# Optimization experiments

Measured on AMD Instinct MI355X. Metric: run time of the kernel, lower is better.

## Reference

```python
import jax, jax.numpy as jnp
import numpy as np

D_IN = 1024
D_OUT = 1024


def setup_inputs() -> dict:
    key = jax.random.key(0)
    kx, kq, kk, kv = jax.random.split(key, 4)
    x = jax.random.normal(kx, (4, 2048, D_IN), dtype=jnp.float32)
    s = 1.0 / np.sqrt(D_IN)
    Wq = jax.random.normal(kq, (D_IN, D_OUT), dtype=jnp.float32) * s
    Wk = jax.random.normal(kk, (D_IN, D_OUT), dtype=jnp.float32) * s
    Wv = jax.random.normal(kv, (D_IN, D_OUT), dtype=jnp.float32) * s
    return {"x": x, "Wq": Wq, "Wk": Wk, "Wv": Wv}


def reference(x, Wq, Wk, Wv):
    # x: [b, s, d_in]; projections [b, s, d_out]
    q = jnp.einsum('bsd,de->bse', x, Wq)
    k = jnp.einsum('bsd,de->bse', x, Wk)
    v = jnp.einsum('bsd,de->bse', x, Wv)
    scale = 1.0 / jnp.sqrt(jnp.asarray(D_OUT, dtype=x.dtype))
    scores = jnp.einsum('bqe,bke->bqk', q, k) * scale  # [b, s, s]
    s_len = x.shape[1]
    causal = jnp.tril(jnp.ones((s_len, s_len), dtype=bool))
    scores = jnp.where(causal[None, :, :], scores, -jnp.inf)
    attn = jax.nn.softmax(scores, axis=-1)
    # dropout p=0.0 -> identity
    return jnp.einsum('bqk,bke->bqe', attn, v)
```

## Files before the change

### kernel.cpp

```cpp
#include <hip/hip_runtime.h>
#include <hip/hip_bf16.h>

#define S_LEN 2048
#define D_DIM 1024
#define NBATCH 4

typedef __attribute__((ext_vector_type(4)))  float f32x4;
typedef __attribute__((ext_vector_type(8)))  short s16x8;
typedef __attribute__((ext_vector_type(4)))  unsigned short u16x4;

__device__ __forceinline__ unsigned short f2b(float f) {
    __hip_bfloat16 h = __float2bfloat16(f);
    return __builtin_bit_cast(unsigned short, h);
}

__device__ __forceinline__ void load_lds16(const unsigned short* g, unsigned short* l) {
    __builtin_amdgcn_global_load_lds(
        (const __attribute__((address_space(1))) void*)(g),
        (__attribute__((address_space(3))) void*)(l), 16, 0, 0);
}

__global__ __launch_bounds__(256)
void cvt_kernel(const float* __restrict__ in, unsigned short* __restrict__ out) {
    long i = ((long)blockIdx.x * 256 + threadIdx.x) * 4;
    f32x4 v = *(const f32x4*)(in + i);
    u16x4 o;
    o.x = f2b(v.x); o.y = f2b(v.y); o.z = f2b(v.z); o.w = f2b(v.w);
    *(u16x4*)(out + i) = o;
}

__global__ __launch_bounds__(256)
void transW_kernel(const float* __restrict__ W0, const float* __restrict__ W1,
                   const float* __restrict__ W2, unsigned short* __restrict__ WT) {
    const float* W = (blockIdx.z == 0) ? W0 : (blockIdx.z == 1) ? W1 : W2;
    unsigned short* O = WT + (long)blockIdx.z * 1024 * 1024;
    __shared__ float t[32][33];
    int tid = threadIdx.x;
    int r  = tid >> 3;
    int c4 = tid & 7;
    int bi = blockIdx.x, bj = blockIdx.y;
    f32x4 v = *(const f32x4*)&W[(long)(bi * 32 + r) * 1024 + bj * 32 + c4 * 4];
    t[r][c4 * 4 + 0] = v.x; t[r][c4 * 4 + 1] = v.y;
    t[r][c4 * 4 + 2] = v.z; t[r][c4 * 4 + 3] = v.w;
    __syncthreads();
    u16x4 o;
    o.x = f2b(t[c4 * 4 + 0][r]); o.y = f2b(t[c4 * 4 + 1][r]);
    o.z = f2b(t[c4 * 4 + 2][r]); o.w = f2b(t[c4 * 4 + 3][r]);
    *(u16x4*)&O[(long)(bj * 32 + r) * 1024 + bi * 32 + c4 * 4] = o;
}

template<int BM, int BN, int OMODE, bool CSKIP, bool CKLIM>
__global__ __launch_bounds__(512, 2)
void gemm_big(const unsigned short* __restrict__ A, int lda, long aStride,
              const unsigned short* __restrict__ Bt, int ldb, long bStride,
              void* __restrict__ Cv, int ldc, long cStride,
              int K, float alpha) {
    constexpr int MF = BM / 32;
    constexpr int NF = BN / 64;
    constexpr int AI = BM / 64;
    constexpr int BI = BN / 64;
    const int bm = blockIdx.x, bn = blockIdx.y, bz = blockIdx.z;
    if (CSKIP && 2 * bn > bm) return;
    A  += (long)bz * aStride;
    Bt += (long)bz * bStride;

    const int tid  = threadIdx.x;
    const int lane = tid & 63;
    const int wid  = tid >> 6;
    const int wm   = wid >> 2;
    const int wn   = wid & 3;

    extern __shared__ __align__(16) unsigned short smem[];
    unsigned short* As = smem;
    unsigned short* Bs = smem + 2 * BM * 64;

    f32x4 acc[MF][NF] = {};

    const int kend = CKLIM ? (bm + 1) * BM : K;
    const int nt   = kend / 64;

    const int srl  = tid >> 3;
    const int sg   = (tid & 7) ^ (srl & 7);
    const int fr   = lane & 15;
    const int fg   = lane >> 4;
    const int rxor = (fr & 7) * 8;

    auto stage = [&](int g) {
        const int k0 = g * 64;
        unsigned short* da = As + (g & 1) * (BM * 64);
        #pragma unroll
        for (int i = 0; i < AI; ++i) {
            const int rl = i * 64 + srl;
            load_lds16(A + (long)(bm * BM + rl) * lda + k0 + sg * 8,
                       da + i * 4096 + wid * 512 + lane * 8);
        }
        unsigned short* db = Bs + (g & 1) * (BN * 64);
        #pragma unroll
        for (int i = 0; i < BI; ++i) {
            const int rl = i * 64 + srl;
            load_lds16(Bt + (long)(bn * BN + rl) * ldb + k0 + sg * 8,
                       db + i * 4096 + wid * 512 + lane * 8);
        }
    };

    stage(0);
    __syncthreads();

    for (int g = 0; g < nt; ++g) {
        if (g + 1 < nt) stage(g + 1);
        const unsigned short* as = As + (g & 1) * (BM * 64);
        const unsigned short* bs = Bs + (g & 1) * (BN * 64);
        #pragma unroll
        for (int ks = 0; ks < 2; ++ks) {
            s16x8 af[MF], bf[NF];
            #pragma unroll
            for (int m = 0; m < MF; ++m) {
                const int row = wm * (BM / 2) + m * 16 + fr;
                af[m] = *(const s16x8*)&as[row * 64 + (((ks * 4 + fg) * 8) ^ rxor)];
            }
            #pragma unroll
            for (int n = 0; n < NF; ++n) {
                const int row = wn * 64 + n * 16 + fr;
                bf[n] = *(const s16x8*)&bs[row * 64 + (((ks * 4 + fg) * 8) ^ rxor)];
            }
            __builtin_amdgcn_s_setprio(1);
            #pragma unroll
            for (int m = 0; m < MF; ++m)
                #pragma unroll
                for (int n = 0; n < NF; ++n)
                    acc[m][n] = __builtin_amdgcn_mfma_f32_16x16x32_bf16(af[m], bf[n], acc[m][n], 0, 0, 0);
            __builtin_amdgcn_s_setprio(0);
        }
        __syncthreads();
    }

    const int crow0 = bm * BM + wm * (BM / 2);
    const int ccol0 = bn * BN + wn * 64;
    const int cr = (lane >> 4) * 4;
    const int cc = lane & 15;
    if (OMODE == 0) {
        unsigned short* C = (unsigned short*)Cv + (long)bz * cStride;
        #pragma unroll
        for (int m = 0; m < MF; ++m)
            #pragma unroll
            for (int r = 0; r < 4; ++r) {
                const long row = crow0 + m * 16 + cr + r;
                #pragma unroll
                for (int n = 0; n < NF; ++n)
                    C[row * ldc + ccol0 + n * 16 + cc] = f2b(acc[m][n][r] * alpha);
            }
    } else {
        float* C = (float*)Cv + (long)bz * cStride;
        #pragma unroll
        for (int m = 0; m < MF; ++m)
            #pragma unroll
            for (int r = 0; r < 4; ++r) {
                const long row = crow0 + m * 16 + cr + r;
                #pragma unroll
                for (int n = 0; n < NF; ++n)
                    C[row * ldc + ccol0 + n * 16 + cc] = acc[m][n][r] * alpha;
            }
    }
}

__global__ __launch_bounds__(256)
void softmax_rows(float* __restrict__ scores) {
    const int i = blockIdx.x;
    const int z = blockIdx.y;
    float* row = scores + ((long)z * S_LEN + i) * S_LEN;
    const int c = i + 1;
    const int tid  = threadIdx.x;
    const int lane = tid & 63;
    const int wid  = tid >> 6;

    f32x4 v0 = ((const f32x4*)row)[tid];
    f32x4 v1 = ((const f32x4*)row)[tid + 256];
    const int j0 = tid * 4, j1 = (tid + 256) * 4;

    float m = -3.4e38f;
    #pragma unroll
    for (int e = 0; e < 4; e++) {
        if (j0 + e < c) m = fmaxf(m, v0[e]);
        if (j1 + e < c) m = fmaxf(m, v1[e]);
    }
    #pragma unroll
    for (int off = 32; off > 0; off >>= 1) m = fmaxf(m, __shfl_xor(m, off));
    __shared__ float redm[4];
    if (lane == 0) redm[wid] = m;
    __syncthreads();
    m = fmaxf(fmaxf(redm[0], redm[1]), fmaxf(redm[2], redm[3]));

    float e0[4], e1[4];
    float s = 0.f;
    #pragma unroll
    for (int e = 0; e < 4; e++) {
        e0[e] = (j0 + e < c) ? __expf(v0[e] - m) : 0.f;
        e1[e] = (j1 + e < c) ? __expf(v1[e] - m) : 0.f;
        s += e0[e] + e1[e];
    }
    #pragma unroll
    for (int off = 32; off > 0; off >>= 1) s += __shfl_xor(s, off);
    __shared__ float reds[4];
    if (lane == 0) reds[wid] = s;
    __syncthreads();
    s = reds[0] + reds[1] + reds[2] + reds[3];
    const float rinv = 1.f / s;

    unsigned short* P = (unsigned short*)row;
    u16x4 o0, o1;
    o0.x = f2b(e0[0] * rinv); o0.y = f2b(e0[1] * rinv);
    o0.z = f2b(e0[2] * rinv); o0.w = f2b(e0[3] * rinv);
    o1.x = f2b(e1[0] * rinv); o1.y = f2b(e1[1] * rinv);
    o1.z = f2b(e1[2] * rinv); o1.w = f2b(e1[3] * rinv);
    *(u16x4*)&P[j0] = o0;
    *(u16x4*)&P[j1] = o1;
}

extern "C" void kernel_launch(void* const* d_in, const int* in_sizes, int n_in,
                              void* d_out, int out_size, void* d_ws, size_t ws_size,
                              hipStream_t stream) {
    const float* x  = (const float*)d_in[0];
    const float* Wq = (const float*)d_in[1];
    const float* Wk = (const float*)d_in[2];
    const float* Wv = (const float*)d_in[3];
    float* out = (float*)d_out;
    char* ws = (char*)d_ws;
    const size_t MiB = 1ull << 20;

    unsigned short* xb  = (unsigned short*)(ws);
    unsigned short* WT  = (unsigned short*)(ws + 16 * MiB);
    unsigned short* Qb  = (unsigned short*)(ws + 22 * MiB);
    unsigned short* Kb  = (unsigned short*)(ws + 38 * MiB);
    unsigned short* VbT = (unsigned short*)(ws + 54 * MiB);
    float* scores       = (float*)(ws + 70 * MiB);

    int nb;
    if      (ws_size >= (70 + 64) * MiB) nb = 4;
    else if (ws_size >= (70 + 32) * MiB) nb = 2;
    else                                 nb = 1;

    const int LDS_QK = 2 * (256 + 256) * 64 * 2;
    const int LDS_SM = 2 * (128 + 256) * 64 * 2;
    hipFuncSetAttribute((const void*)gemm_big<256,256,0,false,false>,
                        hipFuncAttributeMaxDynamicSharedMemorySize, LDS_QK);
    hipFuncSetAttribute((const void*)gemm_big<128,256,0,false,false>,
                        hipFuncAttributeMaxDynamicSharedMemorySize, LDS_SM);
    hipFuncSetAttribute((const void*)gemm_big<128,256,1,true,false>,
                        hipFuncAttributeMaxDynamicSharedMemorySize, LDS_SM);
    hipFuncSetAttribute((const void*)gemm_big<128,256,1,false,true>,
                        hipFuncAttributeMaxDynamicSharedMemorySize, LDS_SM);

    cvt_kernel<<<8192, 256, 0, stream>>>(x, xb);
    transW_kernel<<<dim3(32, 32, 3), 256, 0, stream>>>(Wq, Wk, Wv, WT);

    gemm_big<256,256,0,false,false><<<dim3(32, 4, 2), 512, LDS_QK, stream>>>(
        xb, 1024, 0L, WT, 1024, (long)1024 * 1024,
        Qb, 1024, (long)8192 * 1024, 1024, 1.0f);
    gemm_big<128,256,0,false,false><<<dim3(8, 32, 1), 512, LDS_SM, stream>>>(
        WT + (long)2 * 1024 * 1024, 1024, 0L, xb, 1024, 0L,
        VbT, 8192, 0L, 1024, 1.0f);

    const float alpha = 0.03125f;
    for (int b0 = 0; b0 < NBATCH; b0 += nb) {
        const int nz = (NBATCH - b0 < nb) ? (NBATCH - b0) : nb;
        gemm_big<128,256,1,true,false><<<dim3(16, 8, nz), 512, LDS_SM, stream>>>(
            Qb + (long)b0 * S_LEN * D_DIM, 1024, (long)S_LEN * D_DIM,
            Kb + (long)b0 * S_LEN * D_DIM, 1024, (long)S_LEN * D_DIM,
            scores, S_LEN, (long)S_LEN * S_LEN, 1024, alpha);
        softmax_rows<<<dim3(S_LEN, nz), 256, 0, stream>>>(scores);
        gemm_big<128,256,1,false,true><<<dim3(16, 4, nz), 512, LDS_SM, stream>>>(
            (const unsigned short*)scores, 2 * S_LEN, 2L * S_LEN * S_LEN,
            VbT + (long)b0 * S_LEN, 8192, (long)S_LEN,
            out + (long)b0 * S_LEN * D_DIM, 1024, (long)S_LEN * D_DIM,
            S_LEN, 1.0f);
    }
}
```

Baseline: 242.9 us.

## Triple-buffer GEMM with vmcnt waits, fixed 128x256 tiles, reversed causal block order

Replaces the double-buffered GEMM with a single 128x256 tile kernel that uses a three-stage LDS ring. It waits on outstanding loads with explicit s_waitcnt vmcnt counts plus a single barrier per k-step instead of two syncthreads. The QKV projection moves from 256x256 to 128x256 tiles, and the causal kernels launch the heaviest row blocks first. The aim is deeper overlap of global-to-LDS loads with MFMA work and better load balance, at the cost of 144KB LDS per block, which can reduce occupancy.

Result: no change. 245.9 us (+1.3%).

```diff
diff --git a/kernel.cpp b/kernel.cpp
--- a/kernel.cpp
+++ b/kernel.cpp
@@ -49,17 +49,15 @@
     *(u16x4*)&O[(long)(bj * 32 + r) * 1024 + bi * 32 + c4 * 4] = o;
 }
 
-template<int BM, int BN, int OMODE, bool CSKIP, bool CKLIM>
+template<int OMODE, bool CSKIP, bool CKLIM>
 __global__ __launch_bounds__(512, 2)
-void gemm_big(const unsigned short* __restrict__ A, int lda, long aStride,
+void gemm_cnt(const unsigned short* __restrict__ A, int lda, long aStride,
               const unsigned short* __restrict__ Bt, int ldb, long bStride,
               void* __restrict__ Cv, int ldc, long cStride,
               int K, float alpha) {
-    constexpr int MF = BM / 32;
-    constexpr int NF = BN / 64;
-    constexpr int AI = BM / 64;
-    constexpr int BI = BN / 64;
-    const int bm = blockIdx.x, bn = blockIdx.y, bz = blockIdx.z;
+    constexpr int BUF = (128 + 256) * 64;
+    const int bm = (CSKIP || CKLIM) ? (gridDim.x - 1 - blockIdx.x) : blockIdx.x;
+    const int bn = blockIdx.y, bz = blockIdx.z;
     if (CSKIP && 2 * bn > bm) return;
     A  += (long)bz * aStride;
     Bt += (long)bz * bStride;
@@ -71,93 +69,90 @@
     const int wn   = wid & 3;
 
     extern __shared__ __align__(16) unsigned short smem[];
-    unsigned short* As = smem;
-    unsigned short* Bs = smem + 2 * BM * 64;
-
-    f32x4 acc[MF][NF] = {};
-
-    const int kend = CKLIM ? (bm + 1) * BM : K;
+
+    f32x4 acc[4][4] = {};
+
+    const int kend = CKLIM ? (bm + 1) * 128 : K;
     const int nt   = kend / 64;
 
-    const int srl  = tid >> 3;
-    const int sg   = (tid & 7) ^ (srl & 7);
+    const int srl = tid >> 3;
+    const int sg  = (tid & 7) ^ (srl & 7);
+    const unsigned short* agb = A  + (long)(bm * 128 + srl) * lda + sg * 8;
+    const unsigned short* bgb = Bt + (long)(bn * 256 + srl) * ldb + sg * 8;
+
     const int fr   = lane & 15;
     const int fg   = lane >> 4;
     const int rxor = (fr & 7) * 8;
 
-    auto stage = [&](int g) {
-        const int k0 = g * 64;
-        unsigned short* da = As + (g & 1) * (BM * 64);
-        #pragma unroll
-        for (int i = 0; i < AI; ++i) {
-            const int rl = i * 64 + srl;
-            load_lds16(A + (long)(bm * BM + rl) * lda + k0 + sg * 8,
-                       da + i * 4096 + wid * 512 + lane * 8);
-        }
-        unsigned short* db = Bs + (g & 1) * (BN * 64);
-        #pragma unroll
-        for (int i = 0; i < BI; ++i) {
-            const int rl = i * 64 + srl;
-            load_lds16(Bt + (long)(bn * BN + rl) * ldb + k0 + sg * 8,
-                       db + i * 4096 + wid * 512 + lane * 8);
-        }
+    auto stage = [&](int t) {
+        const int k0 = t * 64;
+        unsigned short* d = smem + (t % 3) * BUF;
+        #pragma unroll
+        for (int i = 0; i < 2; ++i)
+            load_lds16(agb + (long)(i * 64) * lda + k0, d + i * 4096 + tid * 8);
+        #pragma unroll
+        for (int i = 0; i < 4; ++i)
+            load_lds16(bgb + (long)(i * 64) * ldb + k0, d + 8192 + i * 4096 + tid * 8);
     };
 
     stage(0);
-    __syncthreads();
-
-    for (int g = 0; g < nt; ++g) {
-        if (g + 1 < nt) stage(g + 1);
-        const unsigned short* as = As + (g & 1) * (BM * 64);
-        const unsigned short* bs = Bs + (g & 1) * (BN * 64);
+    stage(1);
+
+    for (int t = 0; t < nt; ++t) {
+        if (t + 1 < nt) asm volatile("s_waitcnt vmcnt(6)" ::: "memory");
+        else            asm volatile("s_waitcnt vmcnt(0)" ::: "memory");
+        __builtin_amdgcn_s_barrier();
+        if (t + 2 < nt) stage(t + 2);
+
+        const unsigned short* as = smem + (t % 3) * BUF;
+        const unsigned short* bs = as + 8192;
         #pragma unroll
         for (int ks = 0; ks < 2; ++ks) {
-            s16x8 af[MF], bf[NF];
-            #pragma unroll
-            for (int m = 0; m < MF; ++m) {
-                const int row = wm * (BM / 2) + m * 16 + fr;
+            s16x8 af[4], bf[4];
+            #pragma unroll
+            for (int m = 0; m < 4; ++m) {
+                const int row = wm * 64 + m * 16 + fr;
                 af[m] = *(const s16x8*)&as[row * 64 + (((ks * 4 + fg) * 8) ^ rxor)];
             }
             #pragma unroll
-            for (int n = 0; n < NF; ++n) {
+            for (int n = 0; n < 4; ++n) {
                 const int row = wn * 64 + n * 16 + fr;
                 bf[n] = *(const s16x8*)&bs[row * 64 + (((ks * 4 + fg) * 8) ^ rxor)];
             }
             __builtin_amdgcn_s_setprio(1);
             #pragma unroll
-            for (int m = 0; m < MF; ++m)
+            for (int m = 0; m < 4; ++m)
                 #pragma unroll
-                for (int n = 0; n < NF; ++n)
+                for (int n = 0; n < 4; ++n)
                     acc[m][n] = __builtin_amdgcn_mfma_f32_16x16x32_bf16(af[m], bf[n], acc[m][n], 0, 0, 0);
             __builtin_amdgcn_s_setprio(0);
         }
-        __syncthreads();
-    }
-
-    const int crow0 = bm * BM + wm * (BM / 2);
-    const int ccol0 = bn * BN + wn * 64;
+    }
+
+    const int crow0 = bm * 128 + wm * 64;
+    const int ccol0 = bn * 256 + wn * 64;
     const int cr = (lane >> 4) * 4;
     const int cc = lane & 15;
     if (OMODE == 0) {
         unsigned short* C = (unsigned short*)Cv + (long)bz * cStride;
         #pragma unroll
-        for (int m = 0; m < MF; ++m)
+        for (int m = 0; m < 4; ++m)
             #pragma unroll
             for (int r = 0; r < 4; ++r) {
                 const long row = crow0 + m * 16 + cr + r;
                 #pragma unroll
-                for (int n = 0; n < NF; ++n)
+                for (int n = 0; n < 4; ++n)
                     C[row * ldc + ccol0 + n * 16 + cc] = f2b(acc[m][n][r] * alpha);
             }
     } else {
         float* C = (float*)Cv + (long)bz * cStride;
         #pragma unroll
-        for (int m = 0; m < MF; ++m)
+        for (int m = 0; m < 4; ++m)
             #pragma unroll
             for (int r = 0; r < 4; ++r) {
                 const long row = crow0 + m * 16 + cr + r;
                 #pragma unroll
-                for (int n = 0; n < NF; ++n)
+                for (int n = 0; n < 4; ++n)
                     C[row * ldc + ccol0 + n * 16 + cc] = acc[m][n][r] * alpha;
             }
     }
@@ -239,36 +234,33 @@
     else if (ws_size >= (70 + 32) * MiB) nb = 2;
     else                                 nb = 1;
 
-    const int LDS_QK = 2 * (256 + 256) * 64 * 2;
-    const int LDS_SM = 2 * (128 + 256) * 64 * 2;
-    hipFuncSetAttribute((const void*)gemm_big<256,256,0,false,false>,
-                        hipFuncAttributeMaxDynamicSharedMemorySize, LDS_QK);
-    hipFuncSetAttribute((const void*)gemm_big<128,256,0,false,false>,
-                        hipFuncAttributeMaxDynamicSharedMemorySize, LDS_SM);
-    hipFuncSetAttribute((const void*)gemm_big<128,256,1,true,false>,
-                        hipFuncAttributeMaxDynamicSharedMemorySize, LDS_SM);
-    hipFuncSetAttribute((const void*)gemm_big<128,256,1,false,true>,
-                        hipFuncAttributeMaxDynamicSharedMemorySize, LDS_SM);
+    const int LDS = 3 * (128 + 256) * 64 * 2;
+    hipFuncSetAttribute((const void*)gemm_cnt<0,false,false>,
+                        hipFuncAttributeMaxDynamicSharedMemorySize, LDS);
+    hipFuncSetAttribute((const void*)gemm_cnt<1,true,false>,
+                        hipFuncAttributeMaxDynamicSharedMemorySize, LDS);
+    hipFuncSetAttribute((const void*)gemm_cnt<1,false,true>,
+                        hipFuncAttributeMaxDynamicSharedMemorySize, LDS);
 
     cvt_kernel<<<8192, 256, 0, stream>>>(x, xb);
     transW_kernel<<<dim3(32, 32, 3), 256, 0, stream>>>(Wq, Wk, Wv, WT);
 
-    gemm_big<256,256,0,false,false><<<dim3(32, 4, 2), 512, LDS_QK, stream>>>(
+    gemm_cnt<0,false,false><<<dim3(64, 4, 2), 512, LDS, stream>>>(
         xb, 1024, 0L, WT, 1024, (long)1024 * 1024,
         Qb, 1024, (long)8192 * 1024, 1024, 1.0f);
-    gemm_big<128,256,0,false,false><<<dim3(8, 32, 1), 512, LDS_SM, stream>>>(
+    gemm_cnt<0,false,false><<<dim3(8, 32, 1), 512, LDS, stream>>>(
         WT + (long)2 * 1024 * 1024, 1024, 0L, xb, 1024, 0L,
         VbT, 8192, 0L, 1024, 1.0f);
 
     const float alpha = 0.03125f;
     for (int b0 = 0; b0 < NBATCH; b0 += nb) {
         const int nz = (NBATCH - b0 < nb) ? (NBATCH - b0) : nb;
-        gemm_big<128,256,1,true,false><<<dim3(16, 8, nz), 512, LDS_SM, stream>>>(
+        gemm_cnt<1,true,false><<<dim3(16, 8, nz), 512, LDS, stream>>>(
             Qb + (long)b0 * S_LEN * D_DIM, 1024, (long)S_LEN * D_DIM,
             Kb + (long)b0 * S_LEN * D_DIM, 1024, (long)S_LEN * D_DIM,
             scores, S_LEN, (long)S_LEN * S_LEN, 1024, alpha);
         softmax_rows<<<dim3(S_LEN, nz), 256, 0, stream>>>(scores);
-        gemm_big<128,256,1,false,true><<<dim3(16, 4, nz), 512, LDS_SM, stream>>>(
+        gemm_cnt<1,false,true><<<dim3(16, 4, nz), 512, LDS, stream>>>(
             (const unsigned short*)scores, 2 * S_LEN, 2L * S_LEN * S_LEN,
             VbT + (long)b0 * S_LEN, 8192, (long)S_LEN,
             out + (long)b0 * S_LEN * D_DIM, 1024, (long)S_LEN * D_DIM,
```
